# Kernel optimization log

Hardware: AMD Instinct MI355X
Metric: run time of the kernel (lower is better)

Reference implementation:

```python
import jax, jax.numpy as jnp
import numpy as np

N = 40960   # total nodes per drug branch
E = 131072  # edges per drug branch
B = 1024    # graphs (drug-pair samples)
FXD = 78    # node feature dim
FXT = 37261 # cell-line feature dim
OD = 128    # output_dim


def _lin(k, fi, fo):
    return jax.random.normal(k, (fi, fo), jnp.float32) * 0.02, jnp.zeros((fo,), jnp.float32)


def setup_inputs() -> dict:
    key = jax.random.key(0)
    ks = jax.random.split(key, 16)
    x1 = jax.random.normal(ks[0], (N, FXD), jnp.float32)
    x2 = jax.random.normal(ks[1], (N, FXD), jnp.float32)
    ei1 = jax.random.randint(ks[2], (2, E), 0, N)
    ei2 = jax.random.randint(ks[3], (2, E), 0, N)
    batch = (jnp.arange(N) * B) // N  # sorted graph ids, all B segments non-empty
    cell = jax.random.normal(ks[4], (B, FXT), jnp.float32)
    Wc1, bc1 = _lin(ks[5], FXD, FXD)
    Wc2, bc2 = _lin(ks[6], FXD, FXD * 2)
    Wc3, bc3 = _lin(ks[7], FXD * 2, FXD * 4)
    Wg1, bg1 = _lin(ks[8], FXD * 4, FXD * 2)
    Wg2, bg2 = _lin(ks[9], FXD * 2, OD)
    Wr1, br1 = _lin(ks[10], FXT, 512)
    Wr2, br2 = _lin(ks[11], 512, 256)
    Wr3, br3 = _lin(ks[12], 256, OD)
    Wf1, bf1 = _lin(ks[13], 3 * OD, 512)
    Wf2, bf2 = _lin(ks[14], 512, 128)
    Wo, bo = _lin(ks[15], 128, 2)
    return dict(x1=x1, edge_index1=ei1, batch1=batch, x2=x2, edge_index2=ei2,
                batch2=batch, cell=cell,
                Wc1=Wc1, bc1=bc1, Wc2=Wc2, bc2=bc2, Wc3=Wc3, bc3=bc3,
                Wg1=Wg1, bg1=bg1, Wg2=Wg2, bg2=bg2,
                Wr1=Wr1, br1=br1, Wr2=Wr2, br2=br2, Wr3=Wr3, br3=br3,
                Wf1=Wf1, bf1=bf1, Wf2=Wf2, bf2=bf2, Wo=Wo, bo=bo)


def gcn_conv(x, ei, W, b):
    # PyG GCNConv: add self-loops, symmetric deg^{-1/2} normalization,
    # linear transform, scatter-add aggregation at dst, then bias.
    h = x @ W
    src, dst = ei[0], ei[1]
    deg = jnp.ones((x.shape[0],), h.dtype).at[dst].add(1.0)  # +1 = self loop
    dinv = jax.lax.rsqrt(deg)
    norm = dinv[src] * dinv[dst]
    agg = jnp.zeros_like(h).at[dst].add(h[src] * norm[:, None])
    return agg + h * (dinv * dinv)[:, None] + b  # self-loop norm = 1/deg


def drug_branch(x, ei, batch, Wc1, bc1, Wc2, bc2, Wc3, bc3, Wg1, bg1, Wg2, bg2):
    x = jax.nn.relu(gcn_conv(x, ei, Wc1, bc1))
    x = jax.nn.relu(gcn_conv(x, ei, Wc2, bc2))
    x = jax.nn.relu(gcn_conv(x, ei, Wc3, bc3))
    x = jax.ops.segment_max(x, batch, num_segments=B)  # global max pool
    x = jax.nn.relu(x @ Wg1 + bg1)
    return x @ Wg2 + bg2  # dropout is identity in eval


def reference(x1, edge_index1, batch1, x2, edge_index2, batch2, cell,
              Wc1, bc1, Wc2, bc2, Wc3, bc3, Wg1, bg1, Wg2, bg2,
              Wr1, br1, Wr2, br2, Wr3, br3, Wf1, bf1, Wf2, bf2, Wo, bo):
    # NOTE: the torch code routes x2 through the drug1_* layers too.
    g1 = drug_branch(x1, edge_index1, batch1, Wc1, bc1, Wc2, bc2, Wc3, bc3, Wg1, bg1, Wg2, bg2)
    g2 = drug_branch(x2, edge_index2, batch2, Wc1, bc1, Wc2, bc2, Wc3, bc3, Wg1, bg1, Wg2, bg2)
    cv = cell / jnp.maximum(jnp.linalg.norm(cell, axis=1, keepdims=True), 1e-12)
    cv = jax.nn.relu(cv @ Wr1 + br1)
    cv = jax.nn.relu(cv @ Wr2 + br2)
    cv = cv @ Wr3 + br3
    xc = jnp.concatenate([g1, g2, cv], axis=1)
    xc = jax.nn.relu(xc @ Wf1 + bf1)
    xc = jax.nn.relu(xc @ Wf2 + bf2)
    return xc @ Wo + bo
```

## Files before the change

### kernel.cpp

```cpp
#include <hip/hip_runtime.h>

constexpr int N_NODES = 40960;
constexpr int E_EDGES = 131072;
constexpr int B_GRAPH = 1024;
constexpr int FXD  = 78;
constexpr int FXD2 = 156;
constexpr int FXD4 = 312;
constexpr int OD   = 128;
constexpr int FXT  = 37261;
constexpr int KP   = 37280;
constexpr int NPG  = N_NODES / B_GRAPH;
constexpr int NN2  = 2 * N_NODES;
constexpr int EE2  = 2 * E_EDGES;

typedef unsigned short us16;
typedef __attribute__((ext_vector_type(8))) short short8;
typedef __attribute__((ext_vector_type(4))) float f32x4;

__device__ inline us16 f2bf(float f) {
    unsigned u = __float_as_uint(f);
    return (us16)((u + 0x7FFF + ((u >> 16) & 1)) >> 16);
}
__device__ inline float ldf(const float* p) { return *p; }
__device__ inline float ldf(const us16* p) { return __uint_as_float(((unsigned)*p) << 16); }

__global__ __launch_bounds__(256, 2)
void mfma_cell_gemm(const us16* __restrict__ An, const us16* __restrict__ BwT,
                    const float* __restrict__ ssq, float* __restrict__ C)
{
    __shared__ us16 As[128][40];
    __shared__ us16 Bs[128][40];
    const int tid = threadIdx.x;
    const int m0 = blockIdx.x * 128;
    const int n0 = blockIdx.y * 128;
    const int S  = KP / 32;
    const int per = (S + gridDim.z - 1) / gridDim.z;
    const int s0 = blockIdx.z * per;
    const int s1 = min(S, s0 + per);

    const int r = tid >> 1;
    const int h = (tid & 1) * 16;

    const us16* Ap = An  + (size_t)(m0 + r) * KP + s0 * 32 + h;
    const us16* Bp = BwT + (size_t)(n0 + r) * KP + s0 * 32 + h;

    const int wave = tid >> 6, lane = tid & 63;
    const int wm = (wave >> 1) * 64, wn = (wave & 1) * 64;
    const int fr = lane & 15, fq = (lane >> 4) * 8;

    f32x4 acc[4][4] = {};
    uint4 pa0, pa1, pb0, pb1;
    if (s0 < s1) {
        pa0 = *(const uint4*)Ap;       pa1 = *(const uint4*)(Ap + 8);
        pb0 = *(const uint4*)Bp;       pb1 = *(const uint4*)(Bp + 8);
    }
    for (int s = s0; s < s1; ++s) {
        __syncthreads();
        *(uint4*)&As[r][h] = pa0;  *(uint4*)&As[r][h + 8] = pa1;
        *(uint4*)&Bs[r][h] = pb0;  *(uint4*)&Bs[r][h + 8] = pb1;
        __syncthreads();
        if (s + 1 < s1) {
            Ap += 32; Bp += 32;
            pa0 = *(const uint4*)Ap;  pa1 = *(const uint4*)(Ap + 8);
            pb0 = *(const uint4*)Bp;  pb1 = *(const uint4*)(Bp + 8);
        }
        short8 af[4], bf[4];
#pragma unroll
        for (int t = 0; t < 4; ++t) {
            af[t] = *(const short8*)&As[wm + t * 16 + fr][fq];
            bf[t] = *(const short8*)&Bs[wn + t * 16 + fr][fq];
        }
#pragma unroll
        for (int mt = 0; mt < 4; ++mt)
#pragma unroll
            for (int nt = 0; nt < 4; ++nt)
                acc[mt][nt] = __builtin_amdgcn_mfma_f32_16x16x32_bf16(
                    af[mt], bf[nt], acc[mt][nt], 0, 0, 0);
    }
    float rs[4][4];
#pragma unroll
    for (int mt = 0; mt < 4; ++mt)
#pragma unroll
        for (int reg = 0; reg < 4; ++reg) {
            int row = m0 + wm + mt * 16 + (lane >> 4) * 4 + reg;
            rs[mt][reg] = 1.0f / fmaxf(sqrtf(ssq[row]), 1e-12f);
        }
#pragma unroll
    for (int mt = 0; mt < 4; ++mt)
#pragma unroll
        for (int nt = 0; nt < 4; ++nt)
#pragma unroll
            for (int reg = 0; reg < 4; ++reg) {
                int row = m0 + wm + mt * 16 + (lane >> 4) * 4 + reg;
                int col = n0 + wn + nt * 16 + fr;
                atomicAdd(&C[(size_t)row * 512 + col], acc[mt][nt][reg] * rs[mt][reg]);
            }
}

__global__ __launch_bounds__(256)
void convert_cell_bf(const float* __restrict__ cell, us16* __restrict__ An,
                     float* __restrict__ ssq)
{
    const int row = blockIdx.y;
    const int k8 = (blockIdx.x * 256 + threadIdx.x) * 8;
    const float* src = cell + (size_t)row * FXT;
    float ps = 0.f;
    if (k8 < KP) {
        us16 v[8];
#pragma unroll
        for (int j = 0; j < 8; ++j) {
            int k = k8 + j;
            float x = (k < FXT) ? src[k] : 0.0f;
            ps = fmaf(x, x, ps);
            v[j] = f2bf(x);
        }
        *(uint4*)&An[(size_t)row * KP + k8] = *(uint4*)v;
    }
    for (int off = 32; off > 0; off >>= 1) ps += __shfl_down(ps, off, 64);
    __shared__ float sred[4];
    const int lane = threadIdx.x & 63, wv = threadIdx.x >> 6;
    if (lane == 0) sred[wv] = ps;
    __syncthreads();
    if (threadIdx.x == 0)
        atomicAdd(&ssq[row], sred[0] + sred[1] + sred[2] + sred[3]);
}

__global__ __launch_bounds__(256)
void convert_wT(const float* __restrict__ W, us16* __restrict__ WT,
                int K, int Nn, int KPc)
{
    __shared__ float tile[32][33];
    const int k0 = blockIdx.x * 32;
    const int n0 = blockIdx.y * 32;
    const int c  = threadIdx.x & 31;
    const int r0 = threadIdx.x >> 5;
#pragma unroll
    for (int p = 0; p < 4; ++p) {
        int k = k0 + r0 + p * 8;
        tile[r0 + p * 8][c] = (k < K && n0 + c < Nn) ? W[(size_t)k * Nn + n0 + c] : 0.0f;
    }
    __syncthreads();
#pragma unroll
    for (int p = 0; p < 4; ++p) {
        int n = n0 + r0 + p * 8;
        if (n < Nn) WT[(size_t)n * KPc + k0 + c] = f2bf(tile[c][r0 + p * 8]);
    }
}

__global__ void convert_wT_small(const float* __restrict__ W, us16* __restrict__ WT,
                                 int K, int Nn, int KPc, int NPr)
{
    int idx = blockIdx.x * 256 + threadIdx.x;
    if (idx >= NPr * KPc) return;
    int n = idx / KPc, k = idx - n * KPc;
    WT[idx] = (n < Nn && k < K) ? f2bf(W[(size_t)k * Nn + n]) : (us16)0;
}

template<int KA>
__global__ __launch_bounds__(256, 2)
void mfma_conv(const us16* __restrict__ A, const us16* __restrict__ BT,
               const float* __restrict__ bias, us16* __restrict__ C,
               int Nn, int ldc)
{
    constexpr int KS = KA / 32;
    __shared__ us16 As[2][128][40];
    __shared__ us16 Bs[80][KA + 8];
    const int tid = threadIdx.x;
    const int m0 = blockIdx.x * 128;
    const int n0 = blockIdx.y * 80;

    for (int idx = tid; idx < 80 * (KA / 8); idx += 256) {
        int nr = idx / (KA / 8), c8 = (idx - nr * (KA / 8)) * 8;
        *(uint4*)&Bs[nr][c8] = *(const uint4*)&BT[(size_t)(n0 + nr) * KA + c8];
    }

    const int r = tid >> 1, h = (tid & 1) * 16;
    const us16* Ap = A + (size_t)(m0 + r) * KA + h;
    *(uint4*)&As[0][r][h]     = *(const uint4*)Ap;
    *(uint4*)&As[0][r][h + 8] = *(const uint4*)(Ap + 8);
    __syncthreads();

    const int wave = tid >> 6, lane = tid & 63;
    const int wm = wave * 32;
    const int fr = lane & 15, fq = (lane >> 4) * 8;

    f32x4 acc[2][5] = {};
#pragma unroll
    for (int s = 0; s < KS; ++s) {
        const int cb = s & 1;
        if (s + 1 < KS) {
            uint4 t0 = *(const uint4*)(Ap + 32);
            uint4 t1 = *(const uint4*)(Ap + 40);
            Ap += 32;
            *(uint4*)&As[cb ^ 1][r][h]     = t0;
            *(uint4*)&As[cb ^ 1][r][h + 8] = t1;
        }
        short8 af[2], bf[5];
#pragma unroll
        for (int mt = 0; mt < 2; ++mt)
            af[mt] = *(const short8*)&As[cb][wm + mt * 16 + fr][fq];
#pragma unroll
        for (int nf = 0; nf < 5; ++nf)
            bf[nf] = *(const short8*)&Bs[nf * 16 + fr][s * 32 + fq];
#pragma unroll
        for (int mt = 0; mt < 2; ++mt)
#pragma unroll
            for (int nf = 0; nf < 5; ++nf)
                acc[mt][nf] = __builtin_amdgcn_mfma_f32_16x16x32_bf16(
                    af[mt], bf[nf], acc[mt][nf], 0, 0, 0);
        __syncthreads();
    }

#pragma unroll
    for (int mt = 0; mt < 2; ++mt)
#pragma unroll
        for (int nf = 0; nf < 5; ++nf) {
            const int col = n0 + nf * 16 + fr;
            if (col < Nn) {
                const float bv = bias[col];
#pragma unroll
                for (int reg = 0; reg < 4; ++reg) {
                    int row = m0 + wm + mt * 16 + (lane >> 4) * 4 + reg;
                    C[(size_t)row * ldc + col] = f2bf(fmaxf(acc[mt][nf][reg] + bv, 0.0f));
                }
            }
        }
}

__global__ void deg_count_b(const int* __restrict__ ei1, const int* __restrict__ ei2,
                            int* cnt) {
    int i = blockIdx.x * blockDim.x + threadIdx.x;
    if (i >= EE2) return;
    int d = (i < E_EDGES) ? ei1[E_EDGES + i] : ei2[E_EDGES + (i - E_EDGES)] + N_NODES;
    atomicAdd(&cnt[d], 1);
}

__global__ __launch_bounds__(512)
void scan1(const int* __restrict__ cnt, int* base, int* aux, float* dinv) {
    __shared__ int s[512];
    const int tid = threadIdx.x;
    const int i = blockIdx.x * 512 + tid;
    int v = cnt[i];
    dinv[i] = rsqrtf((float)(v + 1));
    s[tid] = v;
    __syncthreads();
    for (int off = 1; off < 512; off <<= 1) {
        int t = (tid >= off) ? s[tid - off] : 0;
        __syncthreads();
        s[tid] += t;
        __syncthreads();
    }
    base[i] = s[tid] - v;
    if (tid == 511) aux[blockIdx.x] = s[511];
}

__global__ void scan2(int* aux, int nblk) {
    __shared__ int s[256];
    const int tid = threadIdx.x;
    int v = (tid < nblk) ? aux[tid] : 0;
    s[tid] = v;
    __syncthreads();
    for (int off = 1; off < 256; off <<= 1) {
        int t = (tid >= off) ? s[tid - off] : 0;
        __syncthreads();
        s[tid] += t;
        __syncthreads();
    }
    if (tid < nblk) aux[tid] = s[tid] - v;
}

__global__ __launch_bounds__(512)
void scan3(int* base, const int* __restrict__ aux) {
    int i = blockIdx.x * 512 + threadIdx.x;
    base[i] += aux[blockIdx.x];
    if (i == 0) base[NN2] = EE2;
}

__global__ void place_edges_b(const int* __restrict__ ei1, const int* __restrict__ ei2,
                              const float* __restrict__ dinv, const int* __restrict__ base,
                              int* cur, int* __restrict__ esrc, float* __restrict__ enorm) {
    int e = blockIdx.x * blockDim.x + threadIdx.x;
    if (e >= EE2) return;
    int s, d;
    if (e < E_EDGES) { s = ei1[e];            d = ei1[E_EDGES + e]; }
    else             { s = ei2[e - E_EDGES] + N_NODES;
                       d = ei2[E_EDGES + (e - E_EDGES)] + N_NODES; }
    int p = base[d] + atomicAdd(&cur[d], 1);
    esrc[p]  = s;
    enorm[p] = dinv[s] * dinv[d];
}

template<typename Tin, int CH>
__global__ __launch_bounds__(256)
void gather_bf(const Tin* __restrict__ hA, const Tin* __restrict__ hB, int st, int fi, int kaout,
               const float* __restrict__ dinv, const int* __restrict__ base,
               const int* __restrict__ esrc, const float* __restrict__ enorm,
               us16* __restrict__ out)
{
    const int row  = blockIdx.x * 4 + (threadIdx.x >> 6);
    const int lane = threadIdx.x & 63;
    const float d  = dinv[row];
    const float d2 = d * d;
    const Tin* hr = (row < N_NODES) ? hA + (size_t)row * st
                                    : hB + (size_t)(row - N_NODES) * st;
    float acc[CH];
#pragma unroll
    for (int c = 0; c < CH; ++c) {
        int f = lane + 64 * c;
        acc[c] = (f < fi) ? ldf(hr + f) * d2 : 0.0f;
    }
    const int b0 = base[row], b1 = base[row + 1];
    for (int j = b0; j < b1; ++j) {
        const int s = esrc[j];
        const float w = enorm[j];
        const Tin* hs = (s < N_NODES) ? hA + (size_t)s * st
                                      : hB + (size_t)(s - N_NODES) * st;
#pragma unroll
        for (int c = 0; c < CH; ++c) {
            int f = lane + 64 * c;
            if (f < fi) acc[c] = fmaf(ldf(hs + f), w, acc[c]);
        }
    }
    us16* orow = out + (size_t)row * kaout;
#pragma unroll
    for (int c = 0; c < CH; ++c) {
        int f = lane + 64 * c;
        if (f < kaout) orow[f] = f2bf(acc[c]);
    }
}

__global__ void seg_max_bf(const us16* __restrict__ x, float* __restrict__ out,
                           int fo, int ld) {
    int f = blockIdx.x * blockDim.x + threadIdx.x;
    int g = blockIdx.y;
    if (f >= fo) return;
    const us16* xp = x + (size_t)g * NPG * ld + f;
    float v = -1e30f;
#pragma unroll 4
    for (int j = 0; j < NPG; ++j) v = fmaxf(v, ldf(xp + (size_t)j * ld));
    out[(size_t)g * fo + f] = v;
}

template<bool RELU>
__global__ __launch_bounds__(256)
void gemv_rows4(const float* __restrict__ A, const float* __restrict__ B,
                const float* __restrict__ bias, const float* __restrict__ pre,
                float* __restrict__ C, int K, int N, int ldc, int half_off)
{
    __shared__ float As[4 * 512];
    const int tid = threadIdx.x;
    const int r0 = blockIdx.x * 4;
    if (pre) {
        for (int i = tid; i < 4 * K; i += 256)
            As[i] = fmaxf(A[(size_t)r0 * K + i] + pre[i & (K - 1)], 0.0f);
    } else {
        for (int i = tid; i < 4 * K; i += 256) As[i] = A[(size_t)r0 * K + i];
    }
    __syncthreads();
    float* Cb;
    if (half_off != 0)
        Cb = C + (size_t)(r0 & 1023) * ldc + ((r0 >= 1024) ? half_off : 0);
    else
        Cb = C + (size_t)r0 * ldc;
    for (int n = tid; n < N; n += 256) {
        float b0 = bias[n];
        float a0 = b0, a1 = b0, a2 = b0, a3 = b0;
        const float* Bp = B + n;
        for (int k = 0; k < K; ++k) {
            float b = Bp[(size_t)k * N];
            a0 = fmaf(As[k], b, a0);
            a1 = fmaf(As[K + k], b, a1);
            a2 = fmaf(As[2 * K + k], b, a2);
            a3 = fmaf(As[3 * K + k], b, a3);
        }
        if (RELU) { a0 = fmaxf(a0, 0.f); a1 = fmaxf(a1, 0.f); a2 = fmaxf(a2, 0.f); a3 = fmaxf(a3, 0.f); }
        Cb[0 * ldc + n] = a0;
        Cb[1 * ldc + n] = a1;
        Cb[2 * ldc + n] = a2;
        Cb[3 * ldc + n] = a3;
    }
}

__global__ void final_linear2(const float* __restrict__ x, const float* __restrict__ W,
                              const float* __restrict__ b, float* __restrict__ out) {
    int i = blockIdx.x * blockDim.x + threadIdx.x;
    if (i >= B_GRAPH * 2) return;
    int row = i >> 1, o = i & 1;
    const float* xr = x + (size_t)row * 128;
    float acc = b[o];
    for (int k = 0; k < 128; ++k) acc = fmaf(xr[k], W[k * 2 + o], acc);
    out[i] = acc;
}

extern "C" void kernel_launch(void* const* d_in, const int* in_sizes, int n_in,
                              void* d_out, int out_size, void* d_ws, size_t ws_size,
                              hipStream_t stream) {
    (void)in_sizes; (void)n_in; (void)out_size; (void)ws_size;
    const float* x1   = (const float*)d_in[0];
    const int*   ei1  = (const int*)d_in[1];
    const float* x2   = (const float*)d_in[3];
    const int*   ei2  = (const int*)d_in[4];
    const float* cell = (const float*)d_in[6];
    const float* Wc1 = (const float*)d_in[7];  const float* bc1 = (const float*)d_in[8];
    const float* Wc2 = (const float*)d_in[9];  const float* bc2 = (const float*)d_in[10];
    const float* Wc3 = (const float*)d_in[11]; const float* bc3 = (const float*)d_in[12];
    const float* Wg1 = (const float*)d_in[13]; const float* bg1 = (const float*)d_in[14];
    const float* Wg2 = (const float*)d_in[15]; const float* bg2 = (const float*)d_in[16];
    const float* Wr1 = (const float*)d_in[17]; const float* br1 = (const float*)d_in[18];
    const float* Wr2 = (const float*)d_in[19]; const float* br2 = (const float*)d_in[20];
    const float* Wr3 = (const float*)d_in[21]; const float* br3 = (const float*)d_in[22];
    const float* Wf1 = (const float*)d_in[23]; const float* bf1 = (const float*)d_in[24];
    const float* Wf2 = (const float*)d_in[25]; const float* bf2 = (const float*)d_in[26];
    const float* Wo  = (const float*)d_in[27]; const float* bo  = (const float*)d_in[28];
    float* out = (float*)d_out;

    float* ws = (float*)d_ws;
    float* xc   = ws;  ws += (size_t)B_GRAPH * 384;
    float* ssq  = ws;  ws += B_GRAPH;
    float* cv1  = ws;  ws += (size_t)B_GRAPH * 512;
    float* cv2  = ws;  ws += (size_t)B_GRAPH * 256;
    float* f1   = ws;  ws += (size_t)B_GRAPH * 512;
    float* f2   = ws;  ws += (size_t)B_GRAPH * 128;
    float* dinv = ws;  ws += NN2;
    float* pool = ws;  ws += (size_t)2048 * FXD4;
    float* gb   = ws;  ws += (size_t)2048 * FXD2;

    us16* An  = (us16*)ws;
    us16* BwT = An + (size_t)B_GRAPH * KP;

    us16* Abuf = (us16*)ws;
    us16* Hbuf = Abuf + (size_t)NN2 * 160;
    us16* W1T  = Hbuf + (size_t)NN2 * 320;
    us16* W2T  = W1T + 80 * 96;
    us16* W3T  = W2T + 160 * 96;
    float* enorm = (float*)(W3T + 320 * 160);
    int* cnt  = (int*)(enorm + EE2);
    int* cur  = cnt + NN2;
    int* base = cur + NN2;
    int* aux  = base + NN2 + 1;
    int* esrc = aux + 256;

    hipMemsetAsync(ssq, 0, (size_t)B_GRAPH * sizeof(float), stream);
    convert_cell_bf<<<dim3((KP / 8 + 255) / 256, B_GRAPH, 1), 256, 0, stream>>>(cell, An, ssq);
    convert_wT<<<dim3(KP / 32, 512 / 32, 1), 256, 0, stream>>>(Wr1, BwT, FXT, 512, KP);
    hipMemsetAsync(cv1, 0, (size_t)B_GRAPH * 512 * sizeof(float), stream);
    mfma_cell_gemm<<<dim3(8, 4, 32), 256, 0, stream>>>(An, BwT, ssq, cv1);
    gemv_rows4<true><<<B_GRAPH / 4, 256, 0, stream>>>(cv1, Wr2, br2, br1, cv2, 512, 256, 256, 0);
    gemv_rows4<false><<<B_GRAPH / 4, 256, 0, stream>>>(cv2, Wr3, br3, nullptr, xc + 256, 256, OD, 384, 0);

    hipMemsetAsync(cnt, 0, (size_t)2 * NN2 * sizeof(int), stream);
    deg_count_b<<<(EE2 + 255) / 256, 256, 0, stream>>>(ei1, ei2, cnt);
    scan1<<<NN2 / 512, 512, 0, stream>>>(cnt, base, aux, dinv);
    scan2<<<1, 256, 0, stream>>>(aux, NN2 / 512);
    scan3<<<NN2 / 512, 512, 0, stream>>>(base, aux);
    place_edges_b<<<(EE2 + 255) / 256, 256, 0, stream>>>(ei1, ei2, dinv, base, cur, esrc, enorm);

    convert_wT_small<<<(80 * 96 + 255) / 256, 256, 0, stream>>>(Wc1, W1T, FXD, FXD, 96, 80);
    convert_wT_small<<<(160 * 96 + 255) / 256, 256, 0, stream>>>(Wc2, W2T, FXD, FXD2, 96, 160);
    convert_wT_small<<<(320 * 160 + 255) / 256, 256, 0, stream>>>(Wc3, W3T, FXD2, FXD4, 160, 320);

    gather_bf<float, 2><<<NN2 / 4, 256, 0, stream>>>(x1, x2, FXD, FXD, 96,
                                                     dinv, base, esrc, enorm, Abuf);
    mfma_conv<96><<<dim3(NN2 / 128, 1, 1), 256, 0, stream>>>(Abuf, W1T, bc1, Hbuf, FXD, 80);
    gather_bf<us16, 2><<<NN2 / 4, 256, 0, stream>>>(Hbuf, Hbuf + (size_t)N_NODES * 80, 80, FXD, 96,
                                                    dinv, base, esrc, enorm, Abuf);
    mfma_conv<96><<<dim3(NN2 / 128, 2, 1), 256, 0, stream>>>(Abuf, W2T, bc2, Hbuf, FXD2, 160);
    gather_bf<us16, 3><<<NN2 / 4, 256, 0, stream>>>(Hbuf, Hbuf + (size_t)N_NODES * 160, 160, FXD2, 160,
                                                    dinv, base, esrc, enorm, Abuf);
    mfma_conv<160><<<dim3(NN2 / 128, 4, 1), 256, 0, stream>>>(Abuf, W3T, bc3, Hbuf, FXD4, 320);

    seg_max_bf<<<dim3(2, 2048, 1), 256, 0, stream>>>(Hbuf, pool, FXD4, 320);
    gemv_rows4<true><<<2048 / 4, 256, 0, stream>>>(pool, Wg1, bg1, nullptr, gb, FXD4, FXD2, FXD2, 0);
    gemv_rows4<false><<<2048 / 4, 256, 0, stream>>>(gb, Wg2, bg2, nullptr, xc, FXD2, OD, 384, OD);

    gemv_rows4<true><<<B_GRAPH / 4, 256, 0, stream>>>(xc, Wf1, bf1, nullptr, f1, 384, 512, 512, 0);
    gemv_rows4<true><<<B_GRAPH / 4, 256, 0, stream>>>(f1, Wf2, bf2, nullptr, f2, 512, OD, OD, 0);
    final_linear2<<<(B_GRAPH * 2 + 255) / 256, 256, 0, stream>>>(f2, Wo, bo, out);
}
```

Baseline: 1.086 ms.

## Double-buffer cell GEMM with direct global-to-LDS loads and swizzled tiles

Rewrites the bf16 MFMA cell-line GEMM main loop to use global_load_lds async copies into double-buffered, XOR-swizzled shared tiles with a K step of 64. Padding KP grows to a multiple of 64 and the split-K grid shrinks from 32 to 16 slices. The aim is to overlap global loads with MFMA work, cut register staging and bank conflicts, and reduce split-K atomic traffic. In exchange it doubles LDS use per block, which may lower occupancy, and leaves fewer blocks to hide latency.

Measured after the change: 1.048 ms. 3.5% less time.

```diff
diff --git a/kernel.cpp b/kernel.cpp
--- a/kernel.cpp
+++ b/kernel.cpp
@@ -8,7 +8,7 @@
 constexpr int FXD4 = 312;
 constexpr int OD   = 128;
 constexpr int FXT  = 37261;
-constexpr int KP   = 37280;
+constexpr int KP   = 37312;
 constexpr int NPG  = N_NODES / B_GRAPH;
 constexpr int NN2  = 2 * N_NODES;
 constexpr int EE2  = 2 * E_EDGES;
@@ -24,59 +24,74 @@
 __device__ inline float ldf(const float* p) { return *p; }
 __device__ inline float ldf(const us16* p) { return __uint_as_float(((unsigned)*p) << 16); }
 
+#define CG_STAGE(buf, s)                                                       \
+    {                                                                          \
+        _Pragma("unroll")                                                      \
+        for (int i = 0; i < 4; ++i) {                                          \
+            __builtin_amdgcn_global_load_lds(                                  \
+                (const __attribute__((address_space(1))) unsigned*)            \
+                    (Ag + (size_t)i * 8 * KP + (size_t)(s) * 64),              \
+                (__attribute__((address_space(3))) unsigned*)                  \
+                    &As[buf][wave * 32 + i * 8][0], 16, 0, 0);                 \
+            __builtin_amdgcn_global_load_lds(                                  \
+                (const __attribute__((address_space(1))) unsigned*)            \
+                    (Bg + (size_t)i * 8 * KP + (size_t)(s) * 64),              \
+                (__attribute__((address_space(3))) unsigned*)                  \
+                    &Bs[buf][wave * 32 + i * 8][0], 16, 0, 0);                 \
+        }                                                                      \
+    }
+
 __global__ __launch_bounds__(256, 2)
 void mfma_cell_gemm(const us16* __restrict__ An, const us16* __restrict__ BwT,
                     const float* __restrict__ ssq, float* __restrict__ C)
 {
-    __shared__ us16 As[128][40];
-    __shared__ us16 Bs[128][40];
+    __shared__ us16 As[2][128][64];
+    __shared__ us16 Bs[2][128][64];
     const int tid = threadIdx.x;
     const int m0 = blockIdx.x * 128;
     const int n0 = blockIdx.y * 128;
-    const int S  = KP / 32;
+    const int S  = KP / 64;
     const int per = (S + gridDim.z - 1) / gridDim.z;
     const int s0 = blockIdx.z * per;
     const int s1 = min(S, s0 + per);
 
-    const int r = tid >> 1;
-    const int h = (tid & 1) * 16;
-
-    const us16* Ap = An  + (size_t)(m0 + r) * KP + s0 * 32 + h;
-    const us16* Bp = BwT + (size_t)(n0 + r) * KP + s0 * 32 + h;
-
     const int wave = tid >> 6, lane = tid & 63;
+    const int srow = lane >> 3;
+    const int swz  = (lane & 7) ^ srow;
+    const us16* Ag = An  + (size_t)(m0 + wave * 32 + srow) * KP + swz * 8;
+    const us16* Bg = BwT + (size_t)(n0 + wave * 32 + srow) * KP + swz * 8;
+
     const int wm = (wave >> 1) * 64, wn = (wave & 1) * 64;
-    const int fr = lane & 15, fq = (lane >> 4) * 8;
+    const int fr = lane & 15, fq8 = (lane >> 4);
+    const int sx = lane & 7;
 
     f32x4 acc[4][4] = {};
-    uint4 pa0, pa1, pb0, pb1;
-    if (s0 < s1) {
-        pa0 = *(const uint4*)Ap;       pa1 = *(const uint4*)(Ap + 8);
-        pb0 = *(const uint4*)Bp;       pb1 = *(const uint4*)(Bp + 8);
-    }
+
+    CG_STAGE(0, s0)
+    __syncthreads();
+    int cb = 0;
     for (int s = s0; s < s1; ++s) {
-        __syncthreads();
-        *(uint4*)&As[r][h] = pa0;  *(uint4*)&As[r][h + 8] = pa1;
-        *(uint4*)&Bs[r][h] = pb0;  *(uint4*)&Bs[r][h + 8] = pb1;
-        __syncthreads();
-        if (s + 1 < s1) {
-            Ap += 32; Bp += 32;
-            pa0 = *(const uint4*)Ap;  pa1 = *(const uint4*)(Ap + 8);
-            pb0 = *(const uint4*)Bp;  pb1 = *(const uint4*)(Bp + 8);
-        }
-        short8 af[4], bf[4];
-#pragma unroll
-        for (int t = 0; t < 4; ++t) {
-            af[t] = *(const short8*)&As[wm + t * 16 + fr][fq];
-            bf[t] = *(const short8*)&Bs[wn + t * 16 + fr][fq];
-        }
-#pragma unroll
-        for (int mt = 0; mt < 4; ++mt)
-#pragma unroll
-            for (int nt = 0; nt < 4; ++nt)
-                acc[mt][nt] = __builtin_amdgcn_mfma_f32_16x16x32_bf16(
-                    af[mt], bf[nt], acc[mt][nt], 0, 0, 0);
-    }
+        if (s + 1 < s1) CG_STAGE(cb ^ 1, s + 1)
+#pragma unroll
+        for (int ks = 0; ks < 2; ++ks) {
+            const int c = ks * 4 + fq8;
+            short8 af[4], bf[4];
+#pragma unroll
+            for (int t = 0; t < 4; ++t) {
+                af[t] = *(const short8*)&As[cb][wm + t * 16 + fr][(c ^ sx) * 8];
+                bf[t] = *(const short8*)&Bs[cb][wn + t * 16 + fr][(c ^ sx) * 8];
+            }
+#pragma unroll
+            for (int mt = 0; mt < 4; ++mt)
+#pragma unroll
+                for (int nt = 0; nt < 4; ++nt)
+                    acc[mt][nt] = __builtin_amdgcn_mfma_f32_16x16x32_bf16(
+                        af[mt], bf[nt], acc[mt][nt], 0, 0, 0);
+        }
+        __syncthreads();
+        cb ^= 1;
+    }
+
     float rs[4][4];
 #pragma unroll
     for (int mt = 0; mt < 4; ++mt)
@@ -444,7 +459,7 @@
     convert_cell_bf<<<dim3((KP / 8 + 255) / 256, B_GRAPH, 1), 256, 0, stream>>>(cell, An, ssq);
     convert_wT<<<dim3(KP / 32, 512 / 32, 1), 256, 0, stream>>>(Wr1, BwT, FXT, 512, KP);
     hipMemsetAsync(cv1, 0, (size_t)B_GRAPH * 512 * sizeof(float), stream);
-    mfma_cell_gemm<<<dim3(8, 4, 32), 256, 0, stream>>>(An, BwT, ssq, cv1);
+    mfma_cell_gemm<<<dim3(8, 4, 16), 256, 0, stream>>>(An, BwT, ssq, cv1);
     gemv_rows4<true><<<B_GRAPH / 4, 256, 0, stream>>>(cv1, Wr2, br2, br1, cv2, 512, 256, 256, 0);
     gemv_rows4<false><<<B_GRAPH / 4, 256, 0, stream>>>(cv2, Wr3, br3, nullptr, xc + 256, 256, OD, 384, 0);
 
```
